# Performance work log

Hardware: AMD Instinct MI355X
Metric: run time of the kernel (lower is better)

Reference implementation:

```python
import jax, jax.numpy as jnp
import numpy as np

E = 1024   # embed_size
H = 16     # num_heads
D = E // H # head_dim
B, S = 4, 2048

def setup_inputs() -> dict:
    key = jax.random.key(0)
    ks = jax.random.split(key, 11)
    scale = 1.0 / np.sqrt(E)
    inp = {
        "Q": jax.random.normal(ks[0], (B, S, E), jnp.float32),
        "K": jax.random.normal(ks[1], (B, S, E), jnp.float32),
        "V": jax.random.normal(ks[2], (B, S, E), jnp.float32),
        "Wq": jax.random.uniform(ks[3], (E, E), jnp.float32, -scale, scale),
        "bq": jax.random.uniform(ks[4], (E,), jnp.float32, -scale, scale),
        "Wk": jax.random.uniform(ks[5], (E, E), jnp.float32, -scale, scale),
        "bk": jax.random.uniform(ks[6], (E,), jnp.float32, -scale, scale),
        "Wv": jax.random.uniform(ks[7], (E, E), jnp.float32, -scale, scale),
        "bv": jax.random.uniform(ks[8], (E,), jnp.float32, -scale, scale),
        "Wo": jax.random.uniform(ks[9], (E, E), jnp.float32, -scale, scale),
        "bo": jax.random.uniform(ks[10], (E,), jnp.float32, -scale, scale),
    }
    return inp

def reference(Q, K, V, Wq, bq, Wk, bk, Wv, bv, Wo, bo):
    b, sq, _ = Q.shape
    sk = K.shape[1]
    # Linear projections (torch Linear: x @ W.T + b), split into heads -> (b, H, s, D)
    q = (Q @ Wq.T + bq).reshape(b, sq, H, D).transpose(0, 2, 1, 3)
    k = (K @ Wk.T + bk).reshape(b, sk, H, D).transpose(0, 2, 1, 3)
    v = (V @ Wv.T + bv).reshape(b, sk, H, D).transpose(0, 2, 1, 3)
    scores = jnp.einsum('bhqd,bhkd->bhqk', q, k) / jnp.sqrt(jnp.float32(D))
    attn = jax.nn.softmax(scores, axis=-1)
    out = jnp.einsum('bhqk,bhkd->bhqd', attn, v)  # (b, H, sq, D)
    concat = out.transpose(0, 2, 1, 3).reshape(b, sq, E)
    return concat @ Wo.T + bo
```

## Files before the change

### kernel.cpp

```cpp
#include <hip/hip_runtime.h>
#include <hip/hip_bf16.h>

typedef unsigned short u16;
typedef unsigned int u32;
typedef __bf16 bf16x8 __attribute__((ext_vector_type(8)));
typedef float f32x4 __attribute__((ext_vector_type(4)));
typedef float f32x16 __attribute__((ext_vector_type(16)));
typedef unsigned int u32x2 __attribute__((ext_vector_type(2)));

constexpr int E_ = 1024, H_ = 16, D_ = 64, B_ = 4, S_ = 2048;
constexpr int GM = B_ * S_;
constexpr int GN = E_;
constexpr int GK = E_;

__device__ __forceinline__ u16 f2bf(float f) {
  union { float f; u32 u; } v; v.f = f;
  u32 r = v.u + 0x7fffu + ((v.u >> 16) & 1u);
  return (u16)(r >> 16);
}

__device__ __forceinline__ bf16x8 ld_bf16x8(const u16* p) {
  return *reinterpret_cast<const bf16x8*>(p);
}

__device__ __forceinline__ f32x4 mfma16(bf16x8 a, bf16x8 b, f32x4 c) {
  return __builtin_amdgcn_mfma_f32_16x16x32_bf16(a, b, c, 0, 0, 0);
}
__device__ __forceinline__ f32x16 mfma32(bf16x8 a, bf16x8 b, f32x16 c) {
  return __builtin_amdgcn_mfma_f32_32x32x16_bf16(a, b, c, 0, 0, 0);
}

__device__ __forceinline__ u32 cvtpk(float lo, float hi) {
  u32 r;
  asm("v_cvt_pk_bf16_f32 %0, %1, %2" : "=v"(r) : "v"(lo), "v"(hi));
  return r;
}

__device__ __forceinline__ void pl32swap(u32& a, u32& b) {
#if __has_builtin(__builtin_amdgcn_permlane32_swap)
  u32x2 r = __builtin_amdgcn_permlane32_swap(a, b, false, false);
  a = r.x; b = r.y;
#else
  asm volatile("v_permlane32_swap_b32 %0, %1" : "+v"(a), "+v"(b));
#endif
}

__device__ __forceinline__ float fexp2(float x) {
#if __has_builtin(__builtin_amdgcn_exp2f)
  return __builtin_amdgcn_exp2f(x);
#else
  return exp2f(x);
#endif
}

#define GLOAD_LDS16(gp, lp)                                                       \
  __builtin_amdgcn_global_load_lds(                                               \
      (const __attribute__((address_space(1))) u32*)(const void*)(gp),            \
      (__attribute__((address_space(3))) u32*)(void*)(lp), 16, 0, 0)

__global__ __launch_bounds__(256) void cvt7(
    const float4* __restrict__ s0, const float4* __restrict__ s1,
    const float4* __restrict__ s2, const float4* __restrict__ s3,
    const float4* __restrict__ s4, const float4* __restrict__ s5,
    const float4* __restrict__ s6,
    ushort4* __restrict__ d0, ushort4* __restrict__ d1,
    ushort4* __restrict__ d2, ushort4* __restrict__ d3,
    ushort4* __restrict__ d4, ushort4* __restrict__ d5,
    ushort4* __restrict__ d6) {
  long i = (long)blockIdx.x * 256 + threadIdx.x;
  const float4* s; ushort4* d; long j;
  if (i < 2097152L)      { s = s0; d = d0; j = i; }
  else if (i < 4194304L) { s = s1; d = d1; j = i - 2097152L; }
  else if (i < 6291456L) { s = s2; d = d2; j = i - 4194304L; }
  else if (i < 6553600L) { s = s3; d = d3; j = i - 6291456L; }
  else if (i < 6815744L) { s = s4; d = d4; j = i - 6553600L; }
  else if (i < 7077888L) { s = s5; d = d5; j = i - 6815744L; }
  else                   { s = s6; d = d6; j = i - 7077888L; }
  float4 v = s[j];
  ushort4 o;
  o.x = f2bf(v.x); o.y = f2bf(v.y); o.z = f2bf(v.z); o.w = f2bf(v.w);
  d[j] = o;
}

template <int MODE>
__global__ __launch_bounds__(256, 2) void gemm_bt(
    const u16* __restrict__ A, const u16* __restrict__ Bw,
    const float* __restrict__ bias, void* __restrict__ Cout, float scale) {
  __shared__ u16 As[128 * 32];
  __shared__ u16 Bs[128 * 32];
  const int tid = threadIdx.x;
  const int lane = tid & 63, w = tid >> 6;
  const int lr = lane & 15, lg = lane >> 4;
  const int bid = blockIdx.x;
  const int flat = (bid & 7) * 64 + (bid >> 3);
  const int bm = flat >> 3, bn = flat & 7;
  const int wm = (w >> 1) * 64, wn = (w & 1) * 64;

  f32x4 acc[4][4] = {};

  const int byte0 = (w * 2 + 0) * 1024 + lane * 16;
  const int byte1 = (w * 2 + 1) * 1024 + lane * 16;
  const int r0 = byte0 >> 6, c0 = (byte0 & 63) >> 1;
  const int r1 = byte1 >> 6, c1 = (byte1 & 63) >> 1;
  const u16* Arow0 = A + (size_t)(bm * 128 + r0) * GK + c0;
  const u16* Arow1 = A + (size_t)(bm * 128 + r1) * GK + c1;
  const u16* Brow0 = Bw + (size_t)(bn * 128 + r0) * GK + c0;
  const u16* Brow1 = Bw + (size_t)(bn * 128 + r1) * GK + c1;
  u16* As0 = &As[(w * 2 + 0) * 512];
  u16* As1 = &As[(w * 2 + 1) * 512];
  u16* Bs0 = &Bs[(w * 2 + 0) * 512];
  u16* Bs1 = &Bs[(w * 2 + 1) * 512];

  for (int kt = 0; kt < GK / 32; ++kt) {
    const int ko = kt * 32;
    GLOAD_LDS16(Arow0 + ko, As0);
    GLOAD_LDS16(Arow1 + ko, As1);
    GLOAD_LDS16(Brow0 + ko, Bs0);
    GLOAD_LDS16(Brow1 + ko, Bs1);
    __syncthreads();
    bf16x8 af[4], bf_[4];
#pragma unroll
    for (int mi = 0; mi < 4; ++mi)
      af[mi] = ld_bf16x8(&As[(wm + mi * 16 + lr) * 32 + lg * 8]);
#pragma unroll
    for (int ni = 0; ni < 4; ++ni)
      bf_[ni] = ld_bf16x8(&Bs[(wn + ni * 16 + lr) * 32 + lg * 8]);
#pragma unroll
    for (int mi = 0; mi < 4; ++mi)
#pragma unroll
      for (int ni = 0; ni < 4; ++ni)
        acc[mi][ni] = mfma16(af[mi], bf_[ni], acc[mi][ni]);
    __syncthreads();
  }

#pragma unroll
  for (int mi = 0; mi < 4; ++mi)
#pragma unroll
    for (int ni = 0; ni < 4; ++ni) {
      const int n = bn * 128 + wn + ni * 16 + lr;
      const float bv = bias[n];
#pragma unroll
      for (int r = 0; r < 4; ++r) {
        const int m = bm * 128 + wm + mi * 16 + lg * 4 + r;
        const float vv = (acc[mi][ni][r] + bv) * scale;
        if (MODE == 0) {
          const int b = m >> 11, s = m & 2047, h = n >> 6, d = n & 63;
          ((u16*)Cout)[(((size_t)(b * 16 + h) * 2048 + s) * 64) + d] = f2bf(vv);
        } else if (MODE == 1) {
          const int b = m >> 11, s = m & 2047, h = n >> 6, d = n & 63;
          const int bh = b * 16 + h;
          const int t = s >> 6, ks = (s >> 4) & 3, h2 = (s >> 3) & 1, j = s & 7;
          const int dt = d >> 5, lane2 = h2 * 32 + (d & 31);
          ((u16*)Cout)[(size_t)(bh * 32 + t) * 4096 + (dt * 4 + ks) * 512 +
                       lane2 * 8 + j] = f2bf(vv);
        } else {
          ((float*)Cout)[(size_t)m * 1024 + n] = vv;
        }
      }
    }
}

__global__ __launch_bounds__(256, 2) void attn6(
    const u16* __restrict__ q, const u16* __restrict__ k,
    const u16* __restrict__ VB, u16* __restrict__ concat) {
  __shared__ u16 KT[2][64 * 64];
  const int tid = threadIdx.x, lane = tid & 63, w = tid >> 6;
  const int l31 = lane & 31, hi = lane >> 5;
  const int bid = blockIdx.x;
  const int flat = (bid & 7) * 64 + (bid >> 3);
  const int bh = flat >> 3, qt = flat & 7;
  const u16* qbp = q + (size_t)bh * S_ * D_;
  const char* kbase = (const char*)(k + (size_t)bh * S_ * D_);
  const int q0 = qt * 256 + w * 64;

  bf16x8 qf[2][4];
#pragma unroll
  for (int qs = 0; qs < 2; ++qs)
#pragma unroll
    for (int kc = 0; kc < 4; ++kc)
      qf[qs][kc] =
          ld_bf16x8(&qbp[(size_t)(q0 + qs * 32 + l31) * 64 + kc * 16 + hi * 8]);

  f32x16 acc[2][2] = {};
  float l_[2] = {0.f, 0.f};

  const int srow = w * 8 + (lane >> 3);
  const int cswz = (((lane & 7) ^ (lane >> 3)) << 4);
  const char* gk0 = kbase + (size_t)srow * 128 + cswz;
  const char* gk1 = kbase + (size_t)(32 + srow) * 128 + cswz;

  int col4[4];
#pragma unroll
  for (int c = 0; c < 4; ++c)
    col4[c] = (((c * 32 + hi * 16) ^ ((lane & 7) << 4)) >> 1);
  const int rrow = l31 * 64;

  const u16* vbase = VB + (size_t)bh * 32 * 4096 + lane * 8;

#define STAGE(t, buf)                                                     \
  do {                                                                    \
    GLOAD_LDS16(gk0 + (size_t)(t) * 8192, &KT[buf][(0 * 4 + w) * 512]);   \
    GLOAD_LDS16(gk1 + (size_t)(t) * 8192, &KT[buf][(1 * 4 + w) * 512]);   \
  } while (0)

  STAGE(0, 0);
  asm volatile("s_waitcnt vmcnt(0)" ::: "memory");
  __syncthreads();

  for (int t = 0; t < S_ / 64; ++t) {
    const int cur = t & 1, nxt = cur ^ 1;
    if (t < S_ / 64 - 1) STAGE(t + 1, nxt);

    const u16* vb_t = vbase + (size_t)t * 4096;
    bf16x8 vt[2][4];
#pragma unroll
    for (int ks = 0; ks < 4; ++ks) {
      vt[0][ks] = ld_bf16x8(vb_t + ks * 512);
      vt[1][ks] = ld_bf16x8(vb_t + (4 + ks) * 512);
    }

    f32x16 sF[2][2] = {};
#pragma unroll
    for (int st = 0; st < 2; ++st)
#pragma unroll
      for (int kc = 0; kc < 4; ++kc) {
        bf16x8 kf = ld_bf16x8(&KT[cur][st * 2048 + rrow + col4[kc]]);
        sF[0][st] = mfma32(kf, qf[0][kc], sF[0][st]);
        sF[1][st] = mfma32(kf, qf[1][kc], sF[1][st]);
      }

#pragma unroll
    for (int qs = 0; qs < 2; ++qs) {
      float s0 = 0.f, s1 = 0.f, s2 = 0.f, s3 = 0.f;
#pragma unroll
      for (int st = 0; st < 2; ++st)
#pragma unroll
        for (int e = 0; e < 16; e += 4) {
          const float p0 = fexp2(sF[qs][st][e + 0]);
          const float p1 = fexp2(sF[qs][st][e + 1]);
          const float p2 = fexp2(sF[qs][st][e + 2]);
          const float p3 = fexp2(sF[qs][st][e + 3]);
          sF[qs][st][e + 0] = p0; sF[qs][st][e + 1] = p1;
          sF[qs][st][e + 2] = p2; sF[qs][st][e + 3] = p3;
          s0 += p0; s1 += p1; s2 += p2; s3 += p3;
        }
      l_[qs] += (s0 + s1) + (s2 + s3);

#pragma unroll
      for (int ks = 0; ks < 4; ++ks) {
        const int st = ks >> 1, b = (ks & 1) * 8;
        u32 w0 = cvtpk(sF[qs][st][b + 0], sF[qs][st][b + 1]);
        u32 w1 = cvtpk(sF[qs][st][b + 2], sF[qs][st][b + 3]);
        u32 w2 = cvtpk(sF[qs][st][b + 4], sF[qs][st][b + 5]);
        u32 w3 = cvtpk(sF[qs][st][b + 6], sF[qs][st][b + 7]);
        pl32swap(w0, w2);
        pl32swap(w1, w3);
        union { u32 u[4]; bf16x8 v; } pa;
        pa.u[0] = w0; pa.u[1] = w1; pa.u[2] = w2; pa.u[3] = w3;
        acc[qs][0] = mfma32(vt[0][ks], pa.v, acc[qs][0]);
        acc[qs][1] = mfma32(vt[1][ks], pa.v, acc[qs][1]);
      }
    }

    asm volatile("s_waitcnt vmcnt(0)" ::: "memory");
    __syncthreads();
  }
#undef STAGE

  const int b = bh >> 4, h = bh & 15;
#pragma unroll
  for (int qs = 0; qs < 2; ++qs) {
    u32 la = __builtin_bit_cast(u32, l_[qs]), lb = la;
    pl32swap(la, lb);
    const float lt =
        __builtin_bit_cast(float, la) + __builtin_bit_cast(float, lb);
    const float inv = 1.f / lt;
    const int s = q0 + qs * 32 + l31;
    u16* crow = concat + ((size_t)(b * 2048 + s)) * 1024 + h * 64;
#pragma unroll
    for (int dt = 0; dt < 2; ++dt)
#pragma unroll
      for (int g = 0; g < 4; ++g) {
        ushort4 o;
        o.x = f2bf(acc[qs][dt][g * 4 + 0] * inv);
        o.y = f2bf(acc[qs][dt][g * 4 + 1] * inv);
        o.z = f2bf(acc[qs][dt][g * 4 + 2] * inv);
        o.w = f2bf(acc[qs][dt][g * 4 + 3] * inv);
        *(ushort4*)&crow[dt * 32 + g * 8 + hi * 4] = o;
      }
  }
}

extern "C" void kernel_launch(void* const* d_in, const int* in_sizes, int n_in,
                              void* d_out, int out_size, void* d_ws,
                              size_t ws_size, hipStream_t stream) {
  const float* Qf = (const float*)d_in[0];
  const float* Kf = (const float*)d_in[1];
  const float* Vf = (const float*)d_in[2];
  const float* Wq = (const float*)d_in[3];
  const float* bq = (const float*)d_in[4];
  const float* Wk = (const float*)d_in[5];
  const float* bk = (const float*)d_in[6];
  const float* Wv = (const float*)d_in[7];
  const float* bv = (const float*)d_in[8];
  const float* Wo = (const float*)d_in[9];
  const float* bo = (const float*)d_in[10];

  char* ws = (char*)d_ws;
  u16* Xq = (u16*)(ws);
  u16* Xk = Xq + 8388608;
  u16* Xv = Xk + 8388608;
  u16* Wqb = (u16*)(ws + (size_t)3 * 16777216);
  u16* Wkb = Wqb + 1048576;
  u16* Wvb = Wkb + 1048576;
  u16* Wob = Wvb + 1048576;
  u16* qb = (u16*)(ws + (size_t)3 * 16777216 + 8388608);
  u16* kb = qb + (size_t)GM * GN;
  u16* VBb = kb + (size_t)GM * GN;
  u16* concat = Xq;

  cvt7<<<28672, 256, 0, stream>>>(
      (const float4*)Qf, (const float4*)Kf, (const float4*)Vf,
      (const float4*)Wq, (const float4*)Wk, (const float4*)Wv,
      (const float4*)Wo, (ushort4*)Xq, (ushort4*)Xk, (ushort4*)Xv,
      (ushort4*)Wqb, (ushort4*)Wkb, (ushort4*)Wvb, (ushort4*)Wob);

  gemm_bt<0><<<512, 256, 0, stream>>>(Xq, Wqb, bq, qb, 0.18033688011112042f);
  gemm_bt<0><<<512, 256, 0, stream>>>(Xk, Wkb, bk, kb, 1.0f);
  gemm_bt<1><<<512, 256, 0, stream>>>(Xv, Wvb, bv, VBb, 1.0f);

  attn6<<<512, 256, 0, stream>>>(qb, kb, VBb, concat);

  gemm_bt<2><<<512, 256, 0, stream>>>(concat, Wob, bo, (void*)d_out, 1.0f);
}
```

Baseline: 200.7 us.

## Pre-swizzle K into MFMA fragment layout and load directly from global

The K projection GEMM now writes its output in a fragment-ordered layout matching the attention kernel's MFMA operand order, like V already was. The attention kernel drops the LDS double-buffered staging of K along with its per-iteration waitcnt and barrier, and loads K fragments straight from global memory into registers. This removes LDS traffic and block-wide synchronisation, but each wave now fetches K independently from global/L2 (four waves reading the same tile), which raises cache traffic. It also adds more scattered stores to the K GEMM epilogue.

New measurement: 204.7 us. Within noise of the previous version (+2.0%).

```diff
diff --git a/kernel.cpp b/kernel.cpp
--- a/kernel.cpp
+++ b/kernel.cpp
@@ -143,16 +143,21 @@
       for (int r = 0; r < 4; ++r) {
         const int m = bm * 128 + wm + mi * 16 + lg * 4 + r;
         const float vv = (acc[mi][ni][r] + bv) * scale;
+        const int b = m >> 11, s = m & 2047, h = n >> 6, d = n & 63;
         if (MODE == 0) {
-          const int b = m >> 11, s = m & 2047, h = n >> 6, d = n & 63;
           ((u16*)Cout)[(((size_t)(b * 16 + h) * 2048 + s) * 64) + d] = f2bf(vv);
         } else if (MODE == 1) {
-          const int b = m >> 11, s = m & 2047, h = n >> 6, d = n & 63;
           const int bh = b * 16 + h;
           const int t = s >> 6, ks = (s >> 4) & 3, h2 = (s >> 3) & 1, j = s & 7;
           const int dt = d >> 5, lane2 = h2 * 32 + (d & 31);
           ((u16*)Cout)[(size_t)(bh * 32 + t) * 4096 + (dt * 4 + ks) * 512 +
                        lane2 * 8 + j] = f2bf(vv);
+        } else if (MODE == 3) {
+          const int bh = b * 16 + h;
+          const int t = s >> 6, st = (s >> 5) & 1, l31k = s & 31;
+          const int kc = d >> 4, h2 = (d >> 3) & 1, j = d & 7;
+          ((u16*)Cout)[(size_t)(bh * 32 + t) * 4096 + (st * 4 + kc) * 512 +
+                       (h2 * 32 + l31k) * 8 + j] = f2bf(vv);
         } else {
           ((float*)Cout)[(size_t)m * 1024 + n] = vv;
         }
@@ -160,17 +165,15 @@
     }
 }
 
-__global__ __launch_bounds__(256, 2) void attn6(
-    const u16* __restrict__ q, const u16* __restrict__ k,
+__global__ __launch_bounds__(256, 2) void attn9(
+    const u16* __restrict__ q, const u16* __restrict__ KB,
     const u16* __restrict__ VB, u16* __restrict__ concat) {
-  __shared__ u16 KT[2][64 * 64];
   const int tid = threadIdx.x, lane = tid & 63, w = tid >> 6;
   const int l31 = lane & 31, hi = lane >> 5;
   const int bid = blockIdx.x;
   const int flat = (bid & 7) * 64 + (bid >> 3);
   const int bh = flat >> 3, qt = flat & 7;
   const u16* qbp = q + (size_t)bh * S_ * D_;
-  const char* kbase = (const char*)(k + (size_t)bh * S_ * D_);
   const int q0 = qt * 256 + w * 64;
 
   bf16x8 qf[2][4];
@@ -184,39 +187,24 @@
   f32x16 acc[2][2] = {};
   float l_[2] = {0.f, 0.f};
 
-  const int srow = w * 8 + (lane >> 3);
-  const int cswz = (((lane & 7) ^ (lane >> 3)) << 4);
-  const char* gk0 = kbase + (size_t)srow * 128 + cswz;
-  const char* gk1 = kbase + (size_t)(32 + srow) * 128 + cswz;
-
-  int col4[4];
-#pragma unroll
-  for (int c = 0; c < 4; ++c)
-    col4[c] = (((c * 32 + hi * 16) ^ ((lane & 7) << 4)) >> 1);
-  const int rrow = l31 * 64;
-
-  const u16* vbase = VB + (size_t)bh * 32 * 4096 + lane * 8;
-
-#define STAGE(t, buf)                                                     \
-  do {                                                                    \
-    GLOAD_LDS16(gk0 + (size_t)(t) * 8192, &KT[buf][(0 * 4 + w) * 512]);   \
-    GLOAD_LDS16(gk1 + (size_t)(t) * 8192, &KT[buf][(1 * 4 + w) * 512]);   \
-  } while (0)
-
-  STAGE(0, 0);
-  asm volatile("s_waitcnt vmcnt(0)" ::: "memory");
-  __syncthreads();
+  const u16* kbase = KB + (size_t)bh * S_ * D_ + lane * 8;
+  const u16* vbase = VB + (size_t)bh * S_ * D_ + lane * 8;
 
   for (int t = 0; t < S_ / 64; ++t) {
-    const int cur = t & 1, nxt = cur ^ 1;
-    if (t < S_ / 64 - 1) STAGE(t + 1, nxt);
-
+    const u16* kb_t = kbase + (size_t)t * 4096;
     const u16* vb_t = vbase + (size_t)t * 4096;
+
+    bf16x8 kf[2][4];
+#pragma unroll
+    for (int kc = 0; kc < 4; ++kc) {
+      kf[0][kc] = ld_bf16x8(kb_t + (0 * 4 + kc) * 512);
+      kf[1][kc] = ld_bf16x8(kb_t + (1 * 4 + kc) * 512);
+    }
     bf16x8 vt[2][4];
 #pragma unroll
     for (int ks = 0; ks < 4; ++ks) {
-      vt[0][ks] = ld_bf16x8(vb_t + ks * 512);
-      vt[1][ks] = ld_bf16x8(vb_t + (4 + ks) * 512);
+      vt[0][ks] = ld_bf16x8(vb_t + (0 * 4 + ks) * 512);
+      vt[1][ks] = ld_bf16x8(vb_t + (1 * 4 + ks) * 512);
     }
 
     f32x16 sF[2][2] = {};
@@ -224,9 +212,8 @@
     for (int st = 0; st < 2; ++st)
 #pragma unroll
       for (int kc = 0; kc < 4; ++kc) {
-        bf16x8 kf = ld_bf16x8(&KT[cur][st * 2048 + rrow + col4[kc]]);
-        sF[0][st] = mfma32(kf, qf[0][kc], sF[0][st]);
-        sF[1][st] = mfma32(kf, qf[1][kc], sF[1][st]);
+        sF[0][st] = mfma32(kf[st][kc], qf[0][kc], sF[0][st]);
+        sF[1][st] = mfma32(kf[st][kc], qf[1][kc], sF[1][st]);
       }
 
 #pragma unroll
@@ -261,11 +248,7 @@
         acc[qs][1] = mfma32(vt[1][ks], pa.v, acc[qs][1]);
       }
     }
-
-    asm volatile("s_waitcnt vmcnt(0)" ::: "memory");
-    __syncthreads();
   }
-#undef STAGE
 
   const int b = bh >> 4, h = bh & 15;
 #pragma unroll
@@ -315,8 +298,8 @@
   u16* Wvb = Wkb + 1048576;
   u16* Wob = Wvb + 1048576;
   u16* qb = (u16*)(ws + (size_t)3 * 16777216 + 8388608);
-  u16* kb = qb + (size_t)GM * GN;
-  u16* VBb = kb + (size_t)GM * GN;
+  u16* KBb = qb + (size_t)GM * GN;
+  u16* VBb = KBb + (size_t)GM * GN;
   u16* concat = Xq;
 
   cvt7<<<28672, 256, 0, stream>>>(
@@ -326,10 +309,10 @@
       (ushort4*)Wqb, (ushort4*)Wkb, (ushort4*)Wvb, (ushort4*)Wob);
 
   gemm_bt<0><<<512, 256, 0, stream>>>(Xq, Wqb, bq, qb, 0.18033688011112042f);
-  gemm_bt<0><<<512, 256, 0, stream>>>(Xk, Wkb, bk, kb, 1.0f);
+  gemm_bt<3><<<512, 256, 0, stream>>>(Xk, Wkb, bk, KBb, 1.0f);
   gemm_bt<1><<<512, 256, 0, stream>>>(Xv, Wvb, bv, VBb, 1.0f);
 
-  attn6<<<512, 256, 0, stream>>>(qb, kb, VBb, concat);
+  attn9<<<512, 256, 0, stream>>>(qb, KBb, VBb, concat);
 
   gemm_bt<2><<<512, 256, 0, stream>>>(concat, Wob, bo, (void*)d_out, 1.0f);
 }
```
